# Optimization experiments

Measured on AMD Instinct MI355X. Metric: run time of the kernel, lower is better.

Reference implementation:

```python
import jax, jax.numpy as jnp
import numpy as np

B, L, H, G = 16, 1024, 1024, 128


def setup_inputs() -> dict:
    key = jax.random.key(0)
    ks = jax.random.split(key, 6)
    s = 0.02
    return {
        "events": jax.random.normal(ks[0], (B, L, H), jnp.float32),
        "contexts": jax.random.normal(ks[1], (B, L - 1, H), jnp.float32),
        "Wzm": jax.random.normal(ks[2], (2 * H, G), jnp.float32) * s,
        "bzm": jnp.zeros((G,), jnp.float32),
        "Wzv": jax.random.normal(ks[3], (2 * H, G), jnp.float32) * s,
        "bzv": jnp.zeros((G,), jnp.float32),
        "Wqm": jax.random.normal(ks[4], (3 * H, G), jnp.float32) * s,
        "bqm": jnp.zeros((G,), jnp.float32),
        "Wqv": jax.random.normal(ks[5], (3 * H, G), jnp.float32) * s,
        "bqv": jnp.zeros((G,), jnp.float32),
    }


def reference(events, contexts, Wzm, bzm, Wzv, bzv, Wqm, bqm, Wqv, bqv):
    # adjacent event pairs: [B, L-1, 2H]
    ep = jnp.concatenate([events[:, :-1, :], events[:, 1:, :]], axis=-1)
    z_mean = ep @ Wzm + bzm          # [B, L-1, G]
    z_log_var = ep @ Wzv + bzv
    ce = jnp.concatenate([ep, contexts], axis=-1)  # [B, L-1, 3H]
    q_z_mean = ce @ Wqm + bqm
    q_z_log_var = ce @ Wqv + bqv
    # closed-form KL(p || q) for diagonal Gaussians, summed over G per (b, pair)
    kl = 0.5 * jnp.sum(
        q_z_log_var - z_log_var
        + (jnp.exp(z_log_var) + (z_mean - q_z_mean) ** 2) * jnp.exp(-q_z_log_var)
        - 1.0,
        axis=-1,
    )  # [B, L-1]
    kl_loss = jnp.mean(kl).reshape(1)  # sum over (b, pair) / (B * (L-1))
    return (z_mean, z_log_var, q_z_mean, q_z_log_var, kl_loss)
```

## Files before the change

kernel.cpp:

```cpp
#include <hip/hip_runtime.h>
#include <stdint.h>

typedef unsigned short u16;
typedef __attribute__((ext_vector_type(8))) short short8;
typedef __attribute__((ext_vector_type(4))) float f32x4;
typedef __attribute__((ext_vector_type(2))) uint32_t u32x2;

#define B_      16
#define L_      1024
#define H_      1024
#define G_      128
#define M_TOT   16368
#define K_TOT   3072
#define OUT_SEG 2095104
#define KL_IDX  (4*OUT_SEG)
#define KL_BLOCKS 4092

#define WS_WT_OFF    0
#define WS_BIAS_OFF  3145728
#define WS_PART_OFF  3147776

__device__ inline u16 f2bf(float f) {
    union { float f; uint32_t u; } x; x.f = f;
    uint32_t u = x.u;
    return (u16)((u + 0x7fffu + ((u >> 16) & 1u)) >> 16);
}

__device__ inline void gload16(const void* g, void* l) {
    __builtin_amdgcn_global_load_lds(
        (const __attribute__((address_space(1))) void*)g,
        (__attribute__((address_space(3))) void*)l, 16, 0, 0);
}

__global__ __launch_bounds__(256) void prep_kernel(
    const float* __restrict__ Wzm, const float* __restrict__ bzm,
    const float* __restrict__ Wzv, const float* __restrict__ bzv,
    const float* __restrict__ Wqm, const float* __restrict__ bqm,
    const float* __restrict__ Wqv, const float* __restrict__ bqv,
    u16* __restrict__ wt, float* __restrict__ bias)
{
    int n = blockIdx.x;
    int tid = threadIdx.x;
    const float* W; const float* bsrc; int g; int kmax;
    if (n < 128)      { W = Wzm; bsrc = bzm; g = n;       kmax = 2048; }
    else if (n < 256) { W = Wzv; bsrc = bzv; g = n - 128; kmax = 2048; }
    else if (n < 384) { W = Wqm; bsrc = bqm; g = n - 256; kmax = 3072; }
    else              { W = Wqv; bsrc = bqv; g = n - 384; kmax = 3072; }
    if (tid == 0) bias[n] = bsrc[g];
    #pragma unroll
    for (int i = 0; i < 12; ++i) {
        int k = i * 256 + tid;
        float v = (k < kmax) ? W[(size_t)k * G_ + g] : 0.0f;
        wt[(size_t)n * K_TOT + k] = f2bf(v);
    }
}

__global__ __launch_bounds__(256, 2) void gemm_kernel(
    const float* __restrict__ events, const float* __restrict__ contexts,
    const u16* __restrict__ wt, const float* __restrict__ bias,
    float* __restrict__ out)
{
    __shared__ u16 Ab[2][128 * 64];
    __shared__ u16 Bs[2][128 * 64];

    const int tid = threadIdx.x;
    const int bid = blockIdx.x;
    const int xx  = bid & 7;
    const int jj  = bid >> 3;
    const int nb  = jj & 3;
    const int mp  = (jj >> 2) * 8 + xx;
    const int m0  = mp * 128;

    const int lane = tid & 63;
    const int w    = tid >> 6;
    const int wm   = (w >> 1) * 64;
    const int wn   = (w & 1) * 64;
    const int lr   = lane & 15;
    const int kg   = lane >> 4;

    const int r0 = tid >> 2;
    const int q  = tid & 3;
    const float* paE[2]; const float* paC[2];
    int aw[2][4];
    #pragma unroll
    for (int g = 0; g < 2; ++g) {
        int r = r0 + g * 64;
        int m = m0 + r; if (m > M_TOT - 1) m = M_TOT - 1;
        int b = m / 1023;
        int t = m - b * 1023;
        paE[g] = events   + ((size_t)(b * L_ + t)) * H_;
        paC[g] = contexts + ((size_t)(b * (L_ - 1) + t)) * H_;
        #pragma unroll
        for (int j = 0; j < 4; ++j)
            aw[g][j] = r * 64 + (((2 * j + (q >> 1)) ^ (r & 7)) << 3)
                     + (q & 1) * 4;
    }

    const u16* bS[4];
    #pragma unroll
    for (int it = 0; it < 4; ++it) {
        int c  = it * 256 + tid;
        int v  = c >> 3;
        int cs = (c & 7) ^ (v & 7);
        bS[it] = wt + (size_t)(nb * 128 + v) * K_TOT + cs * 8;
    }

    int aoff[4][2], boff[4][2];
    #pragma unroll
    for (int i = 0; i < 4; ++i) {
        int row = wm + i * 16 + lr;
        int nn  = wn + i * 16 + lr;
        #pragma unroll
        for (int ks = 0; ks < 2; ++ks) {
            aoff[i][ks] = row * 64 + (((ks * 4 + kg) ^ (row & 7)) << 3);
            boff[i][ks] = nn  * 64 + (((ks * 4 + kg) ^ (nn  & 7)) << 3);
        }
    }

    f32x4 acc[4][4];
    #pragma unroll
    for (int i = 0; i < 4; ++i)
        #pragma unroll
        for (int j = 0; j < 4; ++j)
            acc[i][j] = (f32x4){0.f, 0.f, 0.f, 0.f};

    auto stageB = [&](int buf, int kt) {
        int k0 = kt * 64;
        #pragma unroll
        for (int it = 0; it < 4; ++it)
            gload16(bS[it] + k0, &Bs[buf][(it * 256 + tid) * 8]);
    };
    auto compute = [&](int buf) {
        #pragma unroll
        for (int ks = 0; ks < 2; ++ks) {
            short8 a[4], bf[4];
            #pragma unroll
            for (int i = 0; i < 4; ++i)
                a[i] = *(const short8*)&Ab[buf][aoff[i][ks]];
            #pragma unroll
            for (int j = 0; j < 4; ++j)
                bf[j] = *(const short8*)&Bs[buf][boff[j][ks]];
            __builtin_amdgcn_s_setprio(1);
            #pragma unroll
            for (int i = 0; i < 4; ++i)
                #pragma unroll
                for (int j = 0; j < 4; ++j)
                    acc[i][j] = __builtin_amdgcn_mfma_f32_16x16x32_bf16(
                        a[i], bf[j], acc[i][j], 0, 0, 0);
            __builtin_amdgcn_s_setprio(0);
        }
    };

    f32x4 P0, P1, P2, P3, P4, P5, P6, P7;
    f32x4 Q0, Q1, Q2, Q3, Q4, Q5, Q6, Q7;

#define LOADA(p, KT)                                                           \
    {                                                                          \
        int k0_ = (KT) * 64;                                                   \
        int rg_ = (KT) >> 4;                                                   \
        int kq_ = (k0_ & 1023) + q * 4;                                        \
        const float* s0_ = (rg_ == 0) ? paE[0]                                 \
                          : (rg_ == 1 ? (paE[0] + H_) : paC[0]);               \
        const float* s1_ = (rg_ == 0) ? paE[1]                                 \
                          : (rg_ == 1 ? (paE[1] + H_) : paC[1]);               \
        s0_ += kq_; s1_ += kq_;                                                \
        p##0 = *(const f32x4*)(s0_ +  0);                                      \
        p##1 = *(const f32x4*)(s0_ + 16);                                      \
        p##2 = *(const f32x4*)(s0_ + 32);                                      \
        p##3 = *(const f32x4*)(s0_ + 48);                                      \
        p##4 = *(const f32x4*)(s1_ +  0);                                      \
        p##5 = *(const f32x4*)(s1_ + 16);                                      \
        p##6 = *(const f32x4*)(s1_ + 32);                                      \
        p##7 = *(const f32x4*)(s1_ + 48);                                      \
    }
#define CVT1(p, RI, G, J, BUF)                                                 \
    {                                                                          \
        uint32_t lo_, hi_;                                                     \
        asm("v_cvt_pk_bf16_f32 %0, %1, %2" : "=v"(lo_) : "v"(p##RI[0]), "v"(p##RI[1])); \
        asm("v_cvt_pk_bf16_f32 %0, %1, %2" : "=v"(hi_) : "v"(p##RI[2]), "v"(p##RI[3])); \
        *(u32x2*)&Ab[BUF][aw[G][J]] = (u32x2){lo_, hi_};                       \
    }
#define CVTW(p, BUF)                                                           \
    CVT1(p, 0, 0, 0, BUF) CVT1(p, 1, 0, 1, BUF)                                \
    CVT1(p, 2, 0, 2, BUF) CVT1(p, 3, 0, 3, BUF)                                \
    CVT1(p, 4, 1, 0, BUF) CVT1(p, 5, 1, 1, BUF)                                \
    CVT1(p, 6, 1, 2, BUF) CVT1(p, 7, 1, 3, BUF)

#define WAITV(N)                                                               \
    asm volatile("s_waitcnt vmcnt(" #N ")" ::: "memory");                      \
    __builtin_amdgcn_sched_barrier(0);
#define LGKM0                                                                  \
    asm volatile("s_waitcnt lgkmcnt(0)" ::: "memory");                         \
    __builtin_amdgcn_sched_barrier(0);
#define BAR __builtin_amdgcn_s_barrier()

    LOADA(P, 0);
    stageB(0, 0);
    WAITV(4);
    CVTW(P, 0);
    LOADA(Q, 1);
    LGKM0;

    for (int t = 0; t < 46; t += 2) {
        LOADA(P, t + 2);
        stageB(1, t + 1);
        WAITV(12); BAR;
        compute(0);
        CVTW(Q, 1);
        LGKM0; BAR;
        LOADA(Q, t + 3);
        stageB(0, t + 2);
        WAITV(12); BAR;
        compute(1);
        CVTW(P, 0);
        LGKM0; BAR;
    }
    stageB(1, 47);
    WAITV(4); BAR;
    compute(0);
    CVTW(Q, 1);
    LGKM0; BAR;
    WAITV(0); BAR;
    compute(1);

#undef LOADA
#undef CVT1
#undef CVTW
#undef WAITV
#undef LGKM0
#undef BAR

    const float* bptr = bias + nb * 128;
    float* obase = out + (size_t)nb * OUT_SEG;
    #pragma unroll
    for (int i = 0; i < 4; ++i) {
        int mloc = wm + i * 16 + kg * 4;
        #pragma unroll
        for (int j = 0; j < 4; ++j) {
            int g = wn + j * 16 + lr;
            float bv = bptr[g];
            #pragma unroll
            for (int rr = 0; rr < 4; ++rr) {
                int mo = m0 + mloc + rr;
                if (mo < M_TOT) obase[(size_t)mo * G_ + g] = acc[i][j][rr] + bv;
            }
        }
    }
}

__global__ __launch_bounds__(256) void kl_kernel(const float* __restrict__ out,
                                                 float* __restrict__ partial)
{
    int wid  = threadIdx.x >> 6;
    int row  = blockIdx.x * 4 + wid;
    int lane = threadIdx.x & 63;
    const float* zm  = out;
    const float* zlv = out + OUT_SEG;
    const float* qm  = out + (size_t)2 * OUT_SEG;
    const float* qlv = out + (size_t)3 * OUT_SEG;
    size_t base = (size_t)row * G_;
    float s = 0.f;
    #pragma unroll
    for (int hh = 0; hh < 2; ++hh) {
        int g = lane + hh * 64;
        float a = zm[base + g], b = zlv[base + g];
        float c = qm[base + g], d = qlv[base + g];
        float diff = a - c;
        s += d - b + (__expf(b) + diff * diff) * __expf(-d) - 1.0f;
    }
    #pragma unroll
    for (int off = 32; off > 0; off >>= 1)
        s += __shfl_down(s, off);
    __shared__ float pw[4];
    if (lane == 0) pw[wid] = s;
    __syncthreads();
    if (threadIdx.x == 0)
        partial[blockIdx.x] = pw[0] + pw[1] + pw[2] + pw[3];
}

__global__ __launch_bounds__(256) void kl_final(const float* __restrict__ partial,
                                                float* __restrict__ out)
{
    float s = 0.f;
    for (int i = threadIdx.x; i < KL_BLOCKS; i += 256) s += partial[i];
    #pragma unroll
    for (int off = 32; off > 0; off >>= 1)
        s += __shfl_down(s, off);
    __shared__ float pw[4];
    int wid = threadIdx.x >> 6;
    int lane = threadIdx.x & 63;
    if (lane == 0) pw[wid] = s;
    __syncthreads();
    if (threadIdx.x == 0)
        out[KL_IDX] = 0.5f * (pw[0] + pw[1] + pw[2] + pw[3]) / (float)M_TOT;
}

extern "C" void kernel_launch(void* const* d_in, const int* in_sizes, int n_in,
                              void* d_out, int out_size, void* d_ws, size_t ws_size,
                              hipStream_t stream)
{
    const float* events   = (const float*)d_in[0];
    const float* contexts = (const float*)d_in[1];
    const float* Wzm = (const float*)d_in[2];
    const float* bzm = (const float*)d_in[3];
    const float* Wzv = (const float*)d_in[4];
    const float* bzv = (const float*)d_in[5];
    const float* Wqm = (const float*)d_in[6];
    const float* bqm = (const float*)d_in[7];
    const float* Wqv = (const float*)d_in[8];
    const float* bqv = (const float*)d_in[9];
    float* out = (float*)d_out;

    u16*   wt      = (u16*)((char*)d_ws + WS_WT_OFF);
    float* bias    = (float*)((char*)d_ws + WS_BIAS_OFF);
    float* partial = (float*)((char*)d_ws + WS_PART_OFF);

    prep_kernel<<<512, 256, 0, stream>>>(Wzm, bzm, Wzv, bzv, Wqm, bqm, Wqv, bqv,
                                         wt, bias);
    gemm_kernel<<<512, 256, 0, stream>>>(events, contexts, wt, bias, out);
    kl_kernel<<<KL_BLOCKS, 256, 0, stream>>>(out, partial);
    kl_final<<<1, 256, 0, stream>>>(partial, out);
}
```

Before: 96.19 us.

## Pre-pack weights into MFMA fragment layout and load B directly to registers

The prep kernel now writes bf16 weights in a k-group-major packed layout, so each lane can load its MFMA B fragment straight from global memory as a 16-byte vector. The GEMM drops the LDS staging buffer for B and its swizzled LDS reads, and double-buffers the B fragments in registers alongside the A prefetch. This removes LDS traffic and LDS footprint for B, at the cost of more VGPRs and every wave fetching its own B fragments from global or L2 memory instead of sharing one staged copy per block.

```diff
diff --git a/kernel.cpp b/kernel.cpp
--- a/kernel.cpp
+++ b/kernel.cpp
@@ -16,7 +16,7 @@
 #define KL_IDX  (4*OUT_SEG)
 #define KL_BLOCKS 4092
 
-#define WS_WT_OFF    0
+#define WS_WTP_OFF   0
 #define WS_BIAS_OFF  3145728
 #define WS_PART_OFF  3147776
 
@@ -24,12 +24,6 @@
     union { float f; uint32_t u; } x; x.f = f;
     uint32_t u = x.u;
     return (u16)((u + 0x7fffu + ((u >> 16) & 1u)) >> 16);
-}
-
-__device__ inline void gload16(const void* g, void* l) {
-    __builtin_amdgcn_global_load_lds(
-        (const __attribute__((address_space(1))) void*)g,
-        (__attribute__((address_space(3))) void*)l, 16, 0, 0);
 }
 
 __global__ __launch_bounds__(256) void prep_kernel(
@@ -37,7 +31,7 @@
     const float* __restrict__ Wzv, const float* __restrict__ bzv,
     const float* __restrict__ Wqm, const float* __restrict__ bqm,
     const float* __restrict__ Wqv, const float* __restrict__ bqv,
-    u16* __restrict__ wt, float* __restrict__ bias)
+    u16* __restrict__ wtp, float* __restrict__ bias)
 {
     int n = blockIdx.x;
     int tid = threadIdx.x;
@@ -51,17 +45,16 @@
     for (int i = 0; i < 12; ++i) {
         int k = i * 256 + tid;
         float v = (k < kmax) ? W[(size_t)k * G_ + g] : 0.0f;
-        wt[(size_t)n * K_TOT + k] = f2bf(v);
+        wtp[(size_t)(k >> 3) * 4096 + n * 8 + (k & 7)] = f2bf(v);
     }
 }
 
 __global__ __launch_bounds__(256, 2) void gemm_kernel(
     const float* __restrict__ events, const float* __restrict__ contexts,
-    const u16* __restrict__ wt, const float* __restrict__ bias,
+    const u16* __restrict__ wtp, const float* __restrict__ bias,
     float* __restrict__ out)
 {
     __shared__ u16 Ab[2][128 * 64];
-    __shared__ u16 Bs[2][128 * 64];
 
     const int tid = threadIdx.x;
     const int bid = blockIdx.x;
@@ -96,25 +89,18 @@
                      + (q & 1) * 4;
     }
 
-    const u16* bS[4];
-    #pragma unroll
-    for (int it = 0; it < 4; ++it) {
-        int c  = it * 256 + tid;
-        int v  = c >> 3;
-        int cs = (c & 7) ^ (v & 7);
-        bS[it] = wt + (size_t)(nb * 128 + v) * K_TOT + cs * 8;
-    }
-
-    int aoff[4][2], boff[4][2];
+    const u16* bb0 = wtp + (size_t)kg * 4096 + (nb * 128 + wn +  0 + lr) * 8;
+    const u16* bb1 = wtp + (size_t)kg * 4096 + (nb * 128 + wn + 16 + lr) * 8;
+    const u16* bb2 = wtp + (size_t)kg * 4096 + (nb * 128 + wn + 32 + lr) * 8;
+    const u16* bb3 = wtp + (size_t)kg * 4096 + (nb * 128 + wn + 48 + lr) * 8;
+
+    int aoff[4][2];
     #pragma unroll
     for (int i = 0; i < 4; ++i) {
         int row = wm + i * 16 + lr;
-        int nn  = wn + i * 16 + lr;
         #pragma unroll
-        for (int ks = 0; ks < 2; ++ks) {
+        for (int ks = 0; ks < 2; ++ks)
             aoff[i][ks] = row * 64 + (((ks * 4 + kg) ^ (row & 7)) << 3);
-            boff[i][ks] = nn  * 64 + (((ks * 4 + kg) ^ (nn  & 7)) << 3);
-        }
     }
 
     f32x4 acc[4][4];
@@ -124,35 +110,24 @@
         for (int j = 0; j < 4; ++j)
             acc[i][j] = (f32x4){0.f, 0.f, 0.f, 0.f};
 
-    auto stageB = [&](int buf, int kt) {
-        int k0 = kt * 64;
-        #pragma unroll
-        for (int it = 0; it < 4; ++it)
-            gload16(bS[it] + k0, &Bs[buf][(it * 256 + tid) * 8]);
-    };
-    auto compute = [&](int buf) {
-        #pragma unroll
-        for (int ks = 0; ks < 2; ++ks) {
-            short8 a[4], bf[4];
-            #pragma unroll
-            for (int i = 0; i < 4; ++i)
-                a[i] = *(const short8*)&Ab[buf][aoff[i][ks]];
-            #pragma unroll
-            for (int j = 0; j < 4; ++j)
-                bf[j] = *(const short8*)&Bs[buf][boff[j][ks]];
-            __builtin_amdgcn_s_setprio(1);
-            #pragma unroll
-            for (int i = 0; i < 4; ++i)
-                #pragma unroll
-                for (int j = 0; j < 4; ++j)
-                    acc[i][j] = __builtin_amdgcn_mfma_f32_16x16x32_bf16(
-                        a[i], bf[j], acc[i][j], 0, 0, 0);
-            __builtin_amdgcn_s_setprio(0);
-        }
-    };
-
     f32x4 P0, P1, P2, P3, P4, P5, P6, P7;
     f32x4 Q0, Q1, Q2, Q3, Q4, Q5, Q6, Q7;
+    short8 BX0, BX1, BX2, BX3, BX4, BX5, BX6, BX7;
+    short8 BY0, BY1, BY2, BY3, BY4, BY5, BY6, BY7;
+
+#define BFRAG(p, KT)                                                           \
+    {                                                                          \
+        const u16* o_ = (const u16*)0 + (size_t)(KT) * 32768;                  \
+        p##0 = *(const short8*)(bb0 + (size_t)(KT) * 32768);                   \
+        p##1 = *(const short8*)(bb0 + (size_t)(KT) * 32768 + 16384);           \
+        p##2 = *(const short8*)(bb1 + (size_t)(KT) * 32768);                   \
+        p##3 = *(const short8*)(bb1 + (size_t)(KT) * 32768 + 16384);           \
+        p##4 = *(const short8*)(bb2 + (size_t)(KT) * 32768);                   \
+        p##5 = *(const short8*)(bb2 + (size_t)(KT) * 32768 + 16384);           \
+        p##6 = *(const short8*)(bb3 + (size_t)(KT) * 32768);                   \
+        p##7 = *(const short8*)(bb3 + (size_t)(KT) * 32768 + 16384);           \
+        (void)o_;                                                              \
+    }
 
 #define LOADA(p, KT)                                                           \
     {                                                                          \
@@ -186,6 +161,57 @@
     CVT1(p, 4, 1, 0, BUF) CVT1(p, 5, 1, 1, BUF)                                \
     CVT1(p, 6, 1, 2, BUF) CVT1(p, 7, 1, 3, BUF)
 
+#define COMPUTE(BUF, p)                                                        \
+    {                                                                          \
+        short8 a0_, a1_, a2_, a3_;                                             \
+                                                                   \
+        a0_ = *(const short8*)&Ab[BUF][aoff[0][0]];                            \
+        a1_ = *(const short8*)&Ab[BUF][aoff[1][0]];                            \
+        a2_ = *(const short8*)&Ab[BUF][aoff[2][0]];                            \
+        a3_ = *(const short8*)&Ab[BUF][aoff[3][0]];                            \
+        __builtin_amdgcn_s_setprio(1);                                         \
+        acc[0][0] = __builtin_amdgcn_mfma_f32_16x16x32_bf16(a0_, p##0, acc[0][0], 0, 0, 0); \
+        acc[0][1] = __builtin_amdgcn_mfma_f32_16x16x32_bf16(a0_, p##2, acc[0][1], 0, 0, 0); \
+        acc[0][2] = __builtin_amdgcn_mfma_f32_16x16x32_bf16(a0_, p##4, acc[0][2], 0, 0, 0); \
+        acc[0][3] = __builtin_amdgcn_mfma_f32_16x16x32_bf16(a0_, p##6, acc[0][3], 0, 0, 0); \
+        acc[1][0] = __builtin_amdgcn_mfma_f32_16x16x32_bf16(a1_, p##0, acc[1][0], 0, 0, 0); \
+        acc[1][1] = __builtin_amdgcn_mfma_f32_16x16x32_bf16(a1_, p##2, acc[1][1], 0, 0, 0); \
+        acc[1][2] = __builtin_amdgcn_mfma_f32_16x16x32_bf16(a1_, p##4, acc[1][2], 0, 0, 0); \
+        acc[1][3] = __builtin_amdgcn_mfma_f32_16x16x32_bf16(a1_, p##6, acc[1][3], 0, 0, 0); \
+        acc[2][0] = __builtin_amdgcn_mfma_f32_16x16x32_bf16(a2_, p##0, acc[2][0], 0, 0, 0); \
+        acc[2][1] = __builtin_amdgcn_mfma_f32_16x16x32_bf16(a2_, p##2, acc[2][1], 0, 0, 0); \
+        acc[2][2] = __builtin_amdgcn_mfma_f32_16x16x32_bf16(a2_, p##4, acc[2][2], 0, 0, 0); \
+        acc[2][3] = __builtin_amdgcn_mfma_f32_16x16x32_bf16(a2_, p##6, acc[2][3], 0, 0, 0); \
+        acc[3][0] = __builtin_amdgcn_mfma_f32_16x16x32_bf16(a3_, p##0, acc[3][0], 0, 0, 0); \
+        acc[3][1] = __builtin_amdgcn_mfma_f32_16x16x32_bf16(a3_, p##2, acc[3][1], 0, 0, 0); \
+        acc[3][2] = __builtin_amdgcn_mfma_f32_16x16x32_bf16(a3_, p##4, acc[3][2], 0, 0, 0); \
+        acc[3][3] = __builtin_amdgcn_mfma_f32_16x16x32_bf16(a3_, p##6, acc[3][3], 0, 0, 0); \
+        __builtin_amdgcn_s_setprio(0);                                         \
+                                                                   \
+        a0_ = *(const short8*)&Ab[BUF][aoff[0][1]];                            \
+        a1_ = *(const short8*)&Ab[BUF][aoff[1][1]];                            \
+        a2_ = *(const short8*)&Ab[BUF][aoff[2][1]];                            \
+        a3_ = *(const short8*)&Ab[BUF][aoff[3][1]];                            \
+        __builtin_amdgcn_s_setprio(1);                                         \
+        acc[0][0] = __builtin_amdgcn_mfma_f32_16x16x32_bf16(a0_, p##1, acc[0][0], 0, 0, 0); \
+        acc[0][1] = __builtin_amdgcn_mfma_f32_16x16x32_bf16(a0_, p##3, acc[0][1], 0, 0, 0); \
+        acc[0][2] = __builtin_amdgcn_mfma_f32_16x16x32_bf16(a0_, p##5, acc[0][2], 0, 0, 0); \
+        acc[0][3] = __builtin_amdgcn_mfma_f32_16x16x32_bf16(a0_, p##7, acc[0][3], 0, 0, 0); \
+        acc[1][0] = __builtin_amdgcn_mfma_f32_16x16x32_bf16(a1_, p##1, acc[1][0], 0, 0, 0); \
+        acc[1][1] = __builtin_amdgcn_mfma_f32_16x16x32_bf16(a1_, p##3, acc[1][1], 0, 0, 0); \
+        acc[1][2] = __builtin_amdgcn_mfma_f32_16x16x32_bf16(a1_, p##5, acc[1][2], 0, 0, 0); \
+        acc[1][3] = __builtin_amdgcn_mfma_f32_16x16x32_bf16(a1_, p##7, acc[1][3], 0, 0, 0); \
+        acc[2][0] = __builtin_amdgcn_mfma_f32_16x16x32_bf16(a2_, p##1, acc[2][0], 0, 0, 0); \
+        acc[2][1] = __builtin_amdgcn_mfma_f32_16x16x32_bf16(a2_, p##3, acc[2][1], 0, 0, 0); \
+        acc[2][2] = __builtin_amdgcn_mfma_f32_16x16x32_bf16(a2_, p##5, acc[2][2], 0, 0, 0); \
+        acc[2][3] = __builtin_amdgcn_mfma_f32_16x16x32_bf16(a2_, p##7, acc[2][3], 0, 0, 0); \
+        acc[3][0] = __builtin_amdgcn_mfma_f32_16x16x32_bf16(a3_, p##1, acc[3][0], 0, 0, 0); \
+        acc[3][1] = __builtin_amdgcn_mfma_f32_16x16x32_bf16(a3_, p##3, acc[3][1], 0, 0, 0); \
+        acc[3][2] = __builtin_amdgcn_mfma_f32_16x16x32_bf16(a3_, p##5, acc[3][2], 0, 0, 0); \
+        acc[3][3] = __builtin_amdgcn_mfma_f32_16x16x32_bf16(a3_, p##7, acc[3][3], 0, 0, 0); \
+        __builtin_amdgcn_s_setprio(0);                                         \
+    }
+
 #define WAITV(N)                                                               \
     asm volatile("s_waitcnt vmcnt(" #N ")" ::: "memory");                      \
     __builtin_amdgcn_sched_barrier(0);
@@ -195,37 +221,40 @@
 #define BAR __builtin_amdgcn_s_barrier()
 
     LOADA(P, 0);
-    stageB(0, 0);
-    WAITV(4);
+    BFRAG(BX, 0);
+    WAITV(8);
     CVTW(P, 0);
     LOADA(Q, 1);
     LGKM0;
+    BAR;
 
     for (int t = 0; t < 46; t += 2) {
+        BFRAG(BY, t + 1);
         LOADA(P, t + 2);
-        stageB(1, t + 1);
-        WAITV(12); BAR;
-        compute(0);
+        WAITV(16); BAR;
+        COMPUTE(0, BX);
         CVTW(Q, 1);
         LGKM0; BAR;
+        BFRAG(BX, t + 2);
         LOADA(Q, t + 3);
-        stageB(0, t + 2);
-        WAITV(12); BAR;
-        compute(1);
+        WAITV(16); BAR;
+        COMPUTE(1, BY);
         CVTW(P, 0);
         LGKM0; BAR;
     }
-    stageB(1, 47);
-    WAITV(4); BAR;
-    compute(0);
+    BFRAG(BY, 47);
+    WAITV(8); BAR;
+    COMPUTE(0, BX);
     CVTW(Q, 1);
     LGKM0; BAR;
-    WAITV(0); BAR;
-    compute(1);
-
+    WAITV(0);
+    COMPUTE(1, BY);
+
+#undef BFRAG
 #undef LOADA
 #undef CVT1
 #undef CVTW
+#undef COMPUTE
 #undef WAITV
 #undef LGKM0
 #undef BAR
@@ -311,13 +340,13 @@
     const float* bqv = (const float*)d_in[9];
     float* out = (float*)d_out;
 
-    u16*   wt      = (u16*)((char*)d_ws + WS_WT_OFF);
+    u16*   wtp     = (u16*)((char*)d_ws + WS_WTP_OFF);
     float* bias    = (float*)((char*)d_ws + WS_BIAS_OFF);
     float* partial = (float*)((char*)d_ws + WS_PART_OFF);
 
     prep_kernel<<<512, 256, 0, stream>>>(Wzm, bzm, Wzv, bzv, Wqm, bqm, Wqv, bqv,
-                                         wt, bias);
-    gemm_kernel<<<512, 256, 0, stream>>>(events, contexts, wt, bias, out);
+                                         wtp, bias);
+    gemm_kernel<<<512, 256, 0, stream>>>(events, contexts, wtp, bias, out);
     kl_kernel<<<KL_BLOCKS, 256, 0, stream>>>(out, partial);
     kl_final<<<1, 256, 0, stream>>>(partial, out);
 }
```

Result: slower. 106.4 us (+10.6%).
